# Kernel tuning notes

Measured on AMD Instinct MI355X. Metric: run time of the kernel, lower is better.

The kernel has to match this reference:

```python
import jax, jax.numpy as jnp
import numpy as np


def setup_inputs() -> dict:
    key = jax.random.key(0)
    k1, k2 = jax.random.split(key)
    B, C, H, W = 1, 256, 96, 96
    C8 = C // 8
    x = jax.random.normal(k1, (B, C, H, W), dtype=jnp.float32)
    # 1x1 conv == per-pixel linear projection; weight [C8, C], bias [C8]
    w_conv = jax.random.normal(k2, (C8, C), dtype=jnp.float32) * (1.0 / np.sqrt(C))
    b_conv = jnp.zeros((C8,), dtype=jnp.float32)
    return {"x": x, "w_conv": w_conv, "b_conv": b_conv}


def reference(x, w_conv, b_conv):
    B, C, H, W = x.shape  # B must be 1 (module constraint)
    C8 = w_conv.shape[0]
    # conv_1: 1x1 conv -> [B, C8, H, W]
    x1 = jnp.einsum('bchw,oc->bohw', x, w_conv) + b_conv[None, :, None, None]
    x1 = x1.reshape(-1, H, W)                      # [C8, H, W] (B=1)
    x2 = x1.transpose(2, 1, 0).reshape(-1, C8)     # [W*H, C8], row idx = w*H + h
    x3 = x1.transpose(0, 2, 1).reshape(-1, W * H)  # [C8, W*H], col idx = w*H + h
    x4 = jax.nn.softmax(x2 @ x3, axis=-1)          # [W*H, W*H]
    x5 = x.reshape(-1, W * H)                      # [C, W*H], col idx = h*W + w
    x6 = jax.nn.softmax(x5 @ x4, axis=-1)          # [C, W*H]
    x7 = x6.reshape(B, C, H, W)
    return jax.nn.softmax(x7 + x, axis=-1)         # softmax over W
```

## Files before the change

kernel.cpp:

```cpp
#include <hip/hip_runtime.h>
#include <math.h>

#define HW 9216
#define NI 18

typedef __attribute__((ext_vector_type(8))) short bf16x8;
typedef __attribute__((ext_vector_type(4))) float f32x4;
typedef unsigned short ushort_t;
typedef unsigned int uint_t;

__device__ __forceinline__ ushort_t f2bf(float f) {
    union { float f; uint_t u; } v; v.f = f;
    uint_t u = v.u + 0x7FFF + ((v.u >> 16) & 1);
    return (ushort_t)(u >> 16);
}

#define BAR() do { asm volatile("s_waitcnt lgkmcnt(0)" ::: "memory"); \
                   __builtin_amdgcn_s_barrier(); } while (0)

__global__ __launch_bounds__(256) void k1_conv(
        const float* __restrict__ x, const float* __restrict__ wc,
        const float* __restrict__ bc, ushort_t* __restrict__ Gbt,
        ushort_t* __restrict__ xtile) {
    __shared__ float wt[256][32];
    __shared__ float red[8][32][33];
    int t = threadIdx.x;
    int jt = blockIdx.x;
    for (int i = t; i < 256 * 32; i += 256) {
        int o = i >> 8, c = i & 255;
        wt[c][o] = wc[i];
    }
    __syncthreads();
    int px = t & 31, cg = t >> 5;
    int n = jt * 32 + px;
    float acc[32];
    #pragma unroll
    for (int o = 0; o < 32; ++o) acc[o] = 0.f;
    int c0 = cg * 32;
    ushort_t* xt_out = &xtile[(size_t)jt * 8192 + px];
    for (int cc = 0; cc < 32; ++cc) {
        int c = c0 + cc;
        float xv = x[c * HW + n];
        xt_out[c * 32] = f2bf(xv);
        #pragma unroll
        for (int o4 = 0; o4 < 8; ++o4) {
            float4 wv = *(const float4*)&wt[c][o4 * 4];
            acc[o4*4+0] = fmaf(wv.x, xv, acc[o4*4+0]);
            acc[o4*4+1] = fmaf(wv.y, xv, acc[o4*4+1]);
            acc[o4*4+2] = fmaf(wv.z, xv, acc[o4*4+2]);
            acc[o4*4+3] = fmaf(wv.w, xv, acc[o4*4+3]);
        }
    }
    #pragma unroll
    for (int o = 0; o < 32; ++o) red[cg][px][o] = acc[o];
    __syncthreads();
    int px2 = t >> 3, o2 = (t & 7) * 4;
    float s[4] = {0.f, 0.f, 0.f, 0.f};
    #pragma unroll
    for (int g = 0; g < 8; ++g) {
        s[0] += red[g][px2][o2 + 0];
        s[1] += red[g][px2][o2 + 1];
        s[2] += red[g][px2][o2 + 2];
        s[3] += red[g][px2][o2 + 3];
    }
    int n2 = jt * 32 + px2;
    int h = n2 / 96, w = n2 % 96;
    int p = w * 96 + h;
    uint2 pk;
    pk.x = (uint_t)f2bf(s[0] + bc[o2+0]) | ((uint_t)f2bf(s[1] + bc[o2+1]) << 16);
    pk.y = (uint_t)f2bf(s[2] + bc[o2+2]) | ((uint_t)f2bf(s[3] + bc[o2+3]) << 16);
    *(uint2*)&Gbt[p * 32 + o2] = pk;
}

__global__ __launch_bounds__(512) void k2_stats(
        const ushort_t* __restrict__ Gbt, float* __restrict__ m_part,
        float* __restrict__ l_part) {
    __shared__ float mred[2][64], lred[2][64];
    int t = threadIdx.x;
    int w = t >> 6, l = t & 63;
    int l15 = l & 15, lg = l >> 4;
    int jb = blockIdx.x % 144, qs = blockIdx.x / 144;
    int j0 = jb * 64;
    int rf = w & 3, qp = w >> 2;
    bf16x8 aj = *(const bf16x8*)&Gbt[(j0 + rf * 16 + l15) * 32 + lg * 8];
    float m[4], lsum[4];
    #pragma unroll
    for (int r = 0; r < 4; ++r) { m[r] = -INFINITY; lsum[r] = 0.f; }
    int qbeg = qs * 1152;
    for (int tq = 0; tq < 18; ++tq) {
        int q0 = qbeg + tq * 64;
        bf16x8 b0 = *(const bf16x8*)&Gbt[(q0 + qp * 32 + l15) * 32 + lg * 8];
        bf16x8 b1 = *(const bf16x8*)&Gbt[(q0 + qp * 32 + 16 + l15) * 32 + lg * 8];
        f32x4 s0 = {0.f,0.f,0.f,0.f}, s1 = {0.f,0.f,0.f,0.f};
        s0 = __builtin_amdgcn_mfma_f32_16x16x32_bf16(aj, b0, s0, 0, 0, 0);
        s1 = __builtin_amdgcn_mfma_f32_16x16x32_bf16(aj, b1, s1, 0, 0, 0);
        #pragma unroll
        for (int r = 0; r < 4; ++r) {
            float tm = fmaxf(s0[r], s1[r]);
            float nm = fmaxf(m[r], tm);
            lsum[r] = lsum[r] * __expf(m[r] - nm)
                    + __expf(s0[r] - nm) + __expf(s1[r] - nm);
            m[r] = nm;
        }
    }
    #pragma unroll
    for (int off = 1; off < 16; off <<= 1) {
        #pragma unroll
        for (int r = 0; r < 4; ++r) {
            float mo = __shfl_xor(m[r], off);
            float lo = __shfl_xor(lsum[r], off);
            float nm = fmaxf(m[r], mo);
            lsum[r] = lsum[r] * __expf(m[r] - nm) + lo * __expf(mo - nm);
            m[r] = nm;
        }
    }
    if (l15 == 0) {
        #pragma unroll
        for (int r = 0; r < 4; ++r) {
            mred[qp][rf * 16 + lg * 4 + r] = m[r];
            lred[qp][rf * 16 + lg * 4 + r] = lsum[r];
        }
    }
    __syncthreads();
    if (t < 64) {
        float m0 = mred[0][t], m1 = mred[1][t];
        float l0 = lred[0][t], l1 = lred[1][t];
        float nm = fmaxf(m0, m1);
        float lv = l0 * __expf(m0 - nm) + l1 * __expf(m1 - nm);
        m_part[qs * HW + j0 + t] = nm;
        l_part[qs * HW + j0 + t] = lv;
    }
}

__global__ __launch_bounds__(256) void k2b_merge(
        const float* __restrict__ m_part, const float* __restrict__ l_part,
        float* __restrict__ mg, float* __restrict__ rlg) {
    int j = blockIdx.x * 256 + threadIdx.x;
    float nm = -INFINITY;
    #pragma unroll
    for (int s = 0; s < 8; ++s) nm = fmaxf(nm, m_part[s * HW + j]);
    float lv = 0.f;
    #pragma unroll
    for (int s = 0; s < 8; ++s)
        lv += l_part[s * HW + j] * __expf(m_part[s * HW + j] - nm);
    mg[j] = nm;
    rlg[j] = 1.0f / lv;
}

__global__ __launch_bounds__(256) void kzero(float* __restrict__ Z) {
    int i = blockIdx.x * 256 + threadIdx.x;
    *(float4*)&Z[i * 4] = make_float4(0.f, 0.f, 0.f, 0.f);
}

__device__ __forceinline__ void phaseA2(
        bf16x8 ap0, bf16x8 ap1, bf16x8 bqA, int p0, int pr0,
        ushort_t* __restrict__ pb, int qc, int l15, int lg,
        const float* __restrict__ mg, const float* __restrict__ rlg) {
    f32x4 s0 = {0.f,0.f,0.f,0.f}, s1 = {0.f,0.f,0.f,0.f};
    s0 = __builtin_amdgcn_mfma_f32_16x16x32_bf16(ap0, bqA, s0, 0, 0, 0);
    s1 = __builtin_amdgcn_mfma_f32_16x16x32_bf16(ap1, bqA, s1, 0, 0, 0);
    int prow0 = p0 + pr0 * 16 + lg * 4;
    int prow1 = prow0 + 16;
    float4 m0 = *(const float4*)&mg[prow0], r0 = *(const float4*)&rlg[prow0];
    float4 m1 = *(const float4*)&mg[prow1], r1 = *(const float4*)&rlg[prow1];
    uint2 pk0, pk1;
    pk0.x = (uint_t)f2bf(__expf(s0[0] - m0.x) * r0.x)
          | ((uint_t)f2bf(__expf(s0[1] - m0.y) * r0.y) << 16);
    pk0.y = (uint_t)f2bf(__expf(s0[2] - m0.z) * r0.z)
          | ((uint_t)f2bf(__expf(s0[3] - m0.w) * r0.w) << 16);
    pk1.x = (uint_t)f2bf(__expf(s1[0] - m1.x) * r1.x)
          | ((uint_t)f2bf(__expf(s1[1] - m1.y) * r1.y) << 16);
    pk1.y = (uint_t)f2bf(__expf(s1[2] - m1.z) * r1.z)
          | ((uint_t)f2bf(__expf(s1[3] - m1.w) * r1.w) << 16);
    ushort_t* row = pb + (qc * 16 + l15) * 72;
    *(uint2*)&row[pr0 * 16 + lg * 4]      = pk0;
    *(uint2*)&row[pr0 * 16 + 16 + lg * 4] = pk1;
}

__global__ __launch_bounds__(512) void k3_pv(
        const ushort_t* __restrict__ xtile, const ushort_t* __restrict__ Gbt,
        const float* __restrict__ mg, const float* __restrict__ rlg,
        float* __restrict__ Z) {
    __shared__ ushort_t Pbt[2][64][72];
    int t = threadIdx.x;
    int w = t >> 6, l = t & 63;
    int l15 = l & 15, lg = l >> 4;
    int qb = blockIdx.x % 144, ps = blockIdx.x / 144;
    int q0 = qb * 64;
    int cg = w & 3, qh = w >> 2;
    int qc = w & 3, pr0 = (w >> 2) * 2;
    bf16x8 bqA = *(const bf16x8*)&Gbt[(q0 + qc * 16 + l15) * 32 + lg * 8];
    f32x4 acc[4][2];
    #pragma unroll
    for (int ci = 0; ci < 4; ++ci)
        #pragma unroll
        for (int qs = 0; qs < 2; ++qs) acc[ci][qs] = (f32x4){0.f,0.f,0.f,0.f};
    int tile0 = ps * (NI * 2);
    int p0beg = ps * (NI * 64);
    {
        bf16x8 ap0 = *(const bf16x8*)&Gbt[(p0beg + pr0 * 16 + l15) * 32 + lg * 8];
        bf16x8 ap1 = *(const bf16x8*)&Gbt[(p0beg + pr0 * 16 + 16 + l15) * 32 + lg * 8];
        phaseA2(ap0, ap1, bqA, p0beg, pr0, &Pbt[0][0][0], qc, l15, lg, mg, rlg);
    }
    bf16x8 apc0 = *(const bf16x8*)&Gbt[(p0beg + 64 + pr0 * 16 + l15) * 32 + lg * 8];
    bf16x8 apc1 = *(const bf16x8*)&Gbt[(p0beg + 64 + pr0 * 16 + 16 + l15) * 32 + lg * 8];
    BAR();

    for (int pt = 0; pt < NI; ++pt) {
        int buf = pt & 1;
        const ushort_t* xt0 =
            &xtile[((size_t)(tile0 + pt * 2) * 256 + cg * 64 + l15) * 32 + lg * 8];
        bf16x8 a00 = *(const bf16x8*)&xt0[0];
        bf16x8 a01 = *(const bf16x8*)&xt0[16 * 32];
        bf16x8 a02 = *(const bf16x8*)&xt0[32 * 32];
        bf16x8 a03 = *(const bf16x8*)&xt0[48 * 32];
        const ushort_t* xt1 = xt0 + 8192;
        bf16x8 a10 = *(const bf16x8*)&xt1[0];
        bf16x8 a11 = *(const bf16x8*)&xt1[16 * 32];
        bf16x8 a12 = *(const bf16x8*)&xt1[32 * 32];
        bf16x8 a13 = *(const bf16x8*)&xt1[48 * 32];
        bf16x8 b00 = *(const bf16x8*)&Pbt[buf][qh * 32 + l15][lg * 8];
        bf16x8 b01 = *(const bf16x8*)&Pbt[buf][qh * 32 + l15][32 + lg * 8];
        bf16x8 b10 = *(const bf16x8*)&Pbt[buf][qh * 32 + 16 + l15][lg * 8];
        bf16x8 b11 = *(const bf16x8*)&Pbt[buf][qh * 32 + 16 + l15][32 + lg * 8];
        if (pt < NI - 1) {
            int p0n = p0beg + (pt + 1) * 64;
            phaseA2(apc0, apc1, bqA, p0n, pr0, &Pbt[buf ^ 1][0][0],
                    qc, l15, lg, mg, rlg);
            int p0nn = p0beg + ((pt < NI - 2) ? (pt + 2) : (NI - 1)) * 64;
            apc0 = *(const bf16x8*)&Gbt[(p0nn + pr0 * 16 + l15) * 32 + lg * 8];
            apc1 = *(const bf16x8*)&Gbt[(p0nn + pr0 * 16 + 16 + l15) * 32 + lg * 8];
        }
        acc[0][0] = __builtin_amdgcn_mfma_f32_16x16x32_bf16(a00, b00, acc[0][0], 0,0,0);
        acc[1][0] = __builtin_amdgcn_mfma_f32_16x16x32_bf16(a01, b00, acc[1][0], 0,0,0);
        acc[2][0] = __builtin_amdgcn_mfma_f32_16x16x32_bf16(a02, b00, acc[2][0], 0,0,0);
        acc[3][0] = __builtin_amdgcn_mfma_f32_16x16x32_bf16(a03, b00, acc[3][0], 0,0,0);
        acc[0][1] = __builtin_amdgcn_mfma_f32_16x16x32_bf16(a00, b10, acc[0][1], 0,0,0);
        acc[1][1] = __builtin_amdgcn_mfma_f32_16x16x32_bf16(a01, b10, acc[1][1], 0,0,0);
        acc[2][1] = __builtin_amdgcn_mfma_f32_16x16x32_bf16(a02, b10, acc[2][1], 0,0,0);
        acc[3][1] = __builtin_amdgcn_mfma_f32_16x16x32_bf16(a03, b10, acc[3][1], 0,0,0);
        acc[0][0] = __builtin_amdgcn_mfma_f32_16x16x32_bf16(a10, b01, acc[0][0], 0,0,0);
        acc[1][0] = __builtin_amdgcn_mfma_f32_16x16x32_bf16(a11, b01, acc[1][0], 0,0,0);
        acc[2][0] = __builtin_amdgcn_mfma_f32_16x16x32_bf16(a12, b01, acc[2][0], 0,0,0);
        acc[3][0] = __builtin_amdgcn_mfma_f32_16x16x32_bf16(a13, b01, acc[3][0], 0,0,0);
        acc[0][1] = __builtin_amdgcn_mfma_f32_16x16x32_bf16(a10, b11, acc[0][1], 0,0,0);
        acc[1][1] = __builtin_amdgcn_mfma_f32_16x16x32_bf16(a11, b11, acc[1][1], 0,0,0);
        acc[2][1] = __builtin_amdgcn_mfma_f32_16x16x32_bf16(a12, b11, acc[2][1], 0,0,0);
        acc[3][1] = __builtin_amdgcn_mfma_f32_16x16x32_bf16(a13, b11, acc[3][1], 0,0,0);
        BAR();
    }
    int qcol = q0 + qh * 32 + l15;
    #pragma unroll
    for (int ci = 0; ci < 4; ++ci) {
        int crow = cg * 64 + ci * 16 + lg * 4;
        #pragma unroll
        for (int r = 0; r < 4; ++r) {
            float* zr = &Z[(size_t)(crow + r) * HW + qcol];
            atomicAdd(zr,      acc[ci][0][r]);
            atomicAdd(zr + 16, acc[ci][1][r]);
        }
    }
}

__global__ __launch_bounds__(512) void k4_softmax(
        const float* __restrict__ x, float* __restrict__ ZO) {
    __shared__ float zrow[HW];
    __shared__ float red[8];
    int t = threadIdx.x, c = blockIdx.x;
    int lane = t & 63, wid = t >> 6;
    const float* Zr = &ZO[(size_t)c * HW];
    float lm = -INFINITY;
    #pragma unroll
    for (int k = 0; k < 18; ++k) {
        float v = Zr[t + 512 * k];
        zrow[t + 512 * k] = v;
        lm = fmaxf(lm, v);
    }
    #pragma unroll
    for (int off = 32; off; off >>= 1) lm = fmaxf(lm, __shfl_xor(lm, off));
    if (lane == 0) red[wid] = lm;
    __syncthreads();
    float M = fmaxf(fmaxf(fmaxf(red[0], red[1]), fmaxf(red[2], red[3])),
                    fmaxf(fmaxf(red[4], red[5]), fmaxf(red[6], red[7])));
    __syncthreads();
    float ls = 0.f;
    #pragma unroll
    for (int k = 0; k < 18; ++k) {
        int i = t + 512 * k;
        float e = __expf(zrow[i] - M);
        zrow[i] = e;
        ls += e;
    }
    #pragma unroll
    for (int off = 32; off; off >>= 1) ls += __shfl_xor(ls, off);
    if (lane == 0) red[wid] = ls;
    __syncthreads();
    float rS = 1.0f / (red[0] + red[1] + red[2] + red[3]
                     + red[4] + red[5] + red[6] + red[7]);
    const float* xr = &x[(size_t)c * HW];
    float* outr = &ZO[(size_t)c * HW];
    for (int kk = 0; kk < 12; ++kk) {
        int h = wid + kk * 8;
        int base = h * 96;
        float v0 = fmaf(zrow[base + lane], rS, xr[base + lane]);
        float v1 = (lane < 32)
                 ? fmaf(zrow[base + 64 + lane], rS, xr[base + 64 + lane])
                 : -INFINITY;
        float mm = fmaxf(v0, v1);
        #pragma unroll
        for (int off = 32; off; off >>= 1) mm = fmaxf(mm, __shfl_xor(mm, off));
        float e0 = __expf(v0 - mm);
        float e1 = (lane < 32) ? __expf(v1 - mm) : 0.f;
        float ss = e0 + e1;
        #pragma unroll
        for (int off = 32; off; off >>= 1) ss += __shfl_xor(ss, off);
        float r = 1.0f / ss;
        outr[base + lane] = e0 * r;
        if (lane < 32) outr[base + 64 + lane] = e1 * r;
    }
}

extern "C" void kernel_launch(void* const* d_in, const int* in_sizes, int n_in,
                              void* d_out, int out_size, void* d_ws, size_t ws_size,
                              hipStream_t stream) {
    const float* x  = (const float*)d_in[0];
    const float* wc = (const float*)d_in[1];
    const float* bc = (const float*)d_in[2];
    float* Z = (float*)d_out;

    float* m_part = (float*)d_ws;
    float* l_part = m_part + 8 * HW;
    float* mg     = l_part + 8 * HW;
    float* rlg    = mg + HW;
    ushort_t* xtile = (ushort_t*)(rlg + HW);
    ushort_t* Gbt   = xtile + 256 * HW;

    k1_conv   <<<288,  256, 0, stream>>>(x, wc, bc, Gbt, xtile);
    k2_stats  <<<1152, 512, 0, stream>>>(Gbt, m_part, l_part);
    k2b_merge <<<36,   256, 0, stream>>>(m_part, l_part, mg, rlg);
    kzero     <<<2304, 256, 0, stream>>>(Z);
    k3_pv     <<<1152, 512, 0, stream>>>(xtile, Gbt, mg, rlg, Z);
    k4_softmax<<<256,  512, 0, stream>>>(x, Z);
}
```

Baseline: 235.7 us.

## Make PV kernel warp-private with barrier-free P tiles and folded softmax scale

The PV kernel now uses 256-thread blocks of 4 waves, each covering 32 query columns. Each wave builds its own P tile in a private LDS slot, so the per-iteration block barriers and the double buffer go away. The softmax max and reciprocal-sum are folded into a single log2-domain offset, so P needs one fma plus exp2 and a packed bf16 convert instruction. The custom zero kernel is replaced with hipMemsetAsync. In exchange, the QK^T recomputation per block doubles (each wave recomputes all 64 p rows for its 32 q columns), the grid doubles, and x-tile loads are duplicated across more blocks.

```diff
diff --git a/kernel.cpp b/kernel.cpp
--- a/kernel.cpp
+++ b/kernel.cpp
@@ -3,6 +3,7 @@
 
 #define HW 9216
 #define NI 18
+#define PROW 72
 
 typedef __attribute__((ext_vector_type(8))) short bf16x8;
 typedef __attribute__((ext_vector_type(4))) float f32x4;
@@ -15,8 +16,15 @@
     return (ushort_t)(u >> 16);
 }
 
-#define BAR() do { asm volatile("s_waitcnt lgkmcnt(0)" ::: "memory"); \
-                   __builtin_amdgcn_s_barrier(); } while (0)
+__device__ __forceinline__ uint_t cvtpk_bf16(float lo, float hi) {
+    uint_t r;
+    asm("v_cvt_pk_bf16_f32 %0, %1, %2" : "=v"(r) : "v"(lo), "v"(hi));
+    return r;
+}
+
+__device__ __forceinline__ float pexp(float s, float mu) {
+    return exp2f(fmaf(s, 1.44269504f, mu));
+}
 
 __global__ __launch_bounds__(256) void k1_conv(
         const float* __restrict__ x, const float* __restrict__ wc,
@@ -134,7 +142,7 @@
 
 __global__ __launch_bounds__(256) void k2b_merge(
         const float* __restrict__ m_part, const float* __restrict__ l_part,
-        float* __restrict__ mg, float* __restrict__ rlg) {
+        float* __restrict__ muS) {
     int j = blockIdx.x * 256 + threadIdx.x;
     float nm = -INFINITY;
     #pragma unroll
@@ -143,119 +151,102 @@
     #pragma unroll
     for (int s = 0; s < 8; ++s)
         lv += l_part[s * HW + j] * __expf(m_part[s * HW + j] - nm);
-    mg[j] = nm;
-    rlg[j] = 1.0f / lv;
-}
-
-__global__ __launch_bounds__(256) void kzero(float* __restrict__ Z) {
-    int i = blockIdx.x * 256 + threadIdx.x;
-    *(float4*)&Z[i * 4] = make_float4(0.f, 0.f, 0.f, 0.f);
-}
-
-__device__ __forceinline__ void phaseA2(
-        bf16x8 ap0, bf16x8 ap1, bf16x8 bqA, int p0, int pr0,
-        ushort_t* __restrict__ pb, int qc, int l15, int lg,
-        const float* __restrict__ mg, const float* __restrict__ rlg) {
-    f32x4 s0 = {0.f,0.f,0.f,0.f}, s1 = {0.f,0.f,0.f,0.f};
-    s0 = __builtin_amdgcn_mfma_f32_16x16x32_bf16(ap0, bqA, s0, 0, 0, 0);
-    s1 = __builtin_amdgcn_mfma_f32_16x16x32_bf16(ap1, bqA, s1, 0, 0, 0);
-    int prow0 = p0 + pr0 * 16 + lg * 4;
-    int prow1 = prow0 + 16;
-    float4 m0 = *(const float4*)&mg[prow0], r0 = *(const float4*)&rlg[prow0];
-    float4 m1 = *(const float4*)&mg[prow1], r1 = *(const float4*)&rlg[prow1];
-    uint2 pk0, pk1;
-    pk0.x = (uint_t)f2bf(__expf(s0[0] - m0.x) * r0.x)
-          | ((uint_t)f2bf(__expf(s0[1] - m0.y) * r0.y) << 16);
-    pk0.y = (uint_t)f2bf(__expf(s0[2] - m0.z) * r0.z)
-          | ((uint_t)f2bf(__expf(s0[3] - m0.w) * r0.w) << 16);
-    pk1.x = (uint_t)f2bf(__expf(s1[0] - m1.x) * r1.x)
-          | ((uint_t)f2bf(__expf(s1[1] - m1.y) * r1.y) << 16);
-    pk1.y = (uint_t)f2bf(__expf(s1[2] - m1.z) * r1.z)
-          | ((uint_t)f2bf(__expf(s1[3] - m1.w) * r1.w) << 16);
-    ushort_t* row = pb + (qc * 16 + l15) * 72;
-    *(uint2*)&row[pr0 * 16 + lg * 4]      = pk0;
-    *(uint2*)&row[pr0 * 16 + 16 + lg * 4] = pk1;
-}
-
-__global__ __launch_bounds__(512) void k3_pv(
+    muS[j] = -(nm + logf(lv)) * 1.44269504f;
+}
+
+__global__ __launch_bounds__(256, 4) void k3_pv(
         const ushort_t* __restrict__ xtile, const ushort_t* __restrict__ Gbt,
-        const float* __restrict__ mg, const float* __restrict__ rlg,
-        float* __restrict__ Z) {
-    __shared__ ushort_t Pbt[2][64][72];
-    int t = threadIdx.x;
-    int w = t >> 6, l = t & 63;
-    int l15 = l & 15, lg = l >> 4;
-    int qb = blockIdx.x % 144, ps = blockIdx.x / 144;
-    int q0 = qb * 64;
-    int cg = w & 3, qh = w >> 2;
-    int qc = w & 3, pr0 = (w >> 2) * 2;
-    bf16x8 bqA = *(const bf16x8*)&Gbt[(q0 + qc * 16 + l15) * 32 + lg * 8];
+        const float* __restrict__ muS, float* __restrict__ Z) {
+    __shared__ ushort_t Pw[4][32][PROW];
+    const int t = threadIdx.x;
+    const int w = t >> 6;
+    const int l15 = t & 15, lg = (t >> 4) & 3;
+    const int qb = blockIdx.x % 288, ps = blockIdx.x / 288;
+    const int q0 = qb * 32;
+    const int cbase = w * 64;
+
+    bf16x8 bq0 = *(const bf16x8*)&Gbt[(q0 + l15) * 32 + lg * 8];
+    bf16x8 bq1 = *(const bf16x8*)&Gbt[(q0 + 16 + l15) * 32 + lg * 8];
+
     f32x4 acc[4][2];
     #pragma unroll
-    for (int ci = 0; ci < 4; ++ci)
-        #pragma unroll
-        for (int qs = 0; qs < 2; ++qs) acc[ci][qs] = (f32x4){0.f,0.f,0.f,0.f};
-    int tile0 = ps * (NI * 2);
-    int p0beg = ps * (NI * 64);
-    {
-        bf16x8 ap0 = *(const bf16x8*)&Gbt[(p0beg + pr0 * 16 + l15) * 32 + lg * 8];
-        bf16x8 ap1 = *(const bf16x8*)&Gbt[(p0beg + pr0 * 16 + 16 + l15) * 32 + lg * 8];
-        phaseA2(ap0, ap1, bqA, p0beg, pr0, &Pbt[0][0][0], qc, l15, lg, mg, rlg);
-    }
-    bf16x8 apc0 = *(const bf16x8*)&Gbt[(p0beg + 64 + pr0 * 16 + l15) * 32 + lg * 8];
-    bf16x8 apc1 = *(const bf16x8*)&Gbt[(p0beg + 64 + pr0 * 16 + 16 + l15) * 32 + lg * 8];
-    BAR();
-
-    for (int pt = 0; pt < NI; ++pt) {
-        int buf = pt & 1;
-        const ushort_t* xt0 =
-            &xtile[((size_t)(tile0 + pt * 2) * 256 + cg * 64 + l15) * 32 + lg * 8];
-        bf16x8 a00 = *(const bf16x8*)&xt0[0];
-        bf16x8 a01 = *(const bf16x8*)&xt0[16 * 32];
-        bf16x8 a02 = *(const bf16x8*)&xt0[32 * 32];
-        bf16x8 a03 = *(const bf16x8*)&xt0[48 * 32];
-        const ushort_t* xt1 = xt0 + 8192;
-        bf16x8 a10 = *(const bf16x8*)&xt1[0];
-        bf16x8 a11 = *(const bf16x8*)&xt1[16 * 32];
-        bf16x8 a12 = *(const bf16x8*)&xt1[32 * 32];
-        bf16x8 a13 = *(const bf16x8*)&xt1[48 * 32];
-        bf16x8 b00 = *(const bf16x8*)&Pbt[buf][qh * 32 + l15][lg * 8];
-        bf16x8 b01 = *(const bf16x8*)&Pbt[buf][qh * 32 + l15][32 + lg * 8];
-        bf16x8 b10 = *(const bf16x8*)&Pbt[buf][qh * 32 + 16 + l15][lg * 8];
-        bf16x8 b11 = *(const bf16x8*)&Pbt[buf][qh * 32 + 16 + l15][32 + lg * 8];
-        if (pt < NI - 1) {
-            int p0n = p0beg + (pt + 1) * 64;
-            phaseA2(apc0, apc1, bqA, p0n, pr0, &Pbt[buf ^ 1][0][0],
-                    qc, l15, lg, mg, rlg);
-            int p0nn = p0beg + ((pt < NI - 2) ? (pt + 2) : (NI - 1)) * 64;
-            apc0 = *(const bf16x8*)&Gbt[(p0nn + pr0 * 16 + l15) * 32 + lg * 8];
-            apc1 = *(const bf16x8*)&Gbt[(p0nn + pr0 * 16 + 16 + l15) * 32 + lg * 8];
-        }
-        acc[0][0] = __builtin_amdgcn_mfma_f32_16x16x32_bf16(a00, b00, acc[0][0], 0,0,0);
-        acc[1][0] = __builtin_amdgcn_mfma_f32_16x16x32_bf16(a01, b00, acc[1][0], 0,0,0);
-        acc[2][0] = __builtin_amdgcn_mfma_f32_16x16x32_bf16(a02, b00, acc[2][0], 0,0,0);
-        acc[3][0] = __builtin_amdgcn_mfma_f32_16x16x32_bf16(a03, b00, acc[3][0], 0,0,0);
-        acc[0][1] = __builtin_amdgcn_mfma_f32_16x16x32_bf16(a00, b10, acc[0][1], 0,0,0);
-        acc[1][1] = __builtin_amdgcn_mfma_f32_16x16x32_bf16(a01, b10, acc[1][1], 0,0,0);
-        acc[2][1] = __builtin_amdgcn_mfma_f32_16x16x32_bf16(a02, b10, acc[2][1], 0,0,0);
-        acc[3][1] = __builtin_amdgcn_mfma_f32_16x16x32_bf16(a03, b10, acc[3][1], 0,0,0);
-        acc[0][0] = __builtin_amdgcn_mfma_f32_16x16x32_bf16(a10, b01, acc[0][0], 0,0,0);
-        acc[1][0] = __builtin_amdgcn_mfma_f32_16x16x32_bf16(a11, b01, acc[1][0], 0,0,0);
-        acc[2][0] = __builtin_amdgcn_mfma_f32_16x16x32_bf16(a12, b01, acc[2][0], 0,0,0);
-        acc[3][0] = __builtin_amdgcn_mfma_f32_16x16x32_bf16(a13, b01, acc[3][0], 0,0,0);
-        acc[0][1] = __builtin_amdgcn_mfma_f32_16x16x32_bf16(a10, b11, acc[0][1], 0,0,0);
-        acc[1][1] = __builtin_amdgcn_mfma_f32_16x16x32_bf16(a11, b11, acc[1][1], 0,0,0);
-        acc[2][1] = __builtin_amdgcn_mfma_f32_16x16x32_bf16(a12, b11, acc[2][1], 0,0,0);
-        acc[3][1] = __builtin_amdgcn_mfma_f32_16x16x32_bf16(a13, b11, acc[3][1], 0,0,0);
-        BAR();
-    }
-    int qcol = q0 + qh * 32 + l15;
-    #pragma unroll
     for (int ci = 0; ci < 4; ++ci) {
-        int crow = cg * 64 + ci * 16 + lg * 4;
+        acc[ci][0] = (f32x4){0.f,0.f,0.f,0.f};
+        acc[ci][1] = (f32x4){0.f,0.f,0.f,0.f};
+    }
+
+    const int p0beg = ps * (NI * 64);
+    const int tile0 = ps * (NI * 2);
+    ushort_t* pw = &Pw[w][0][0];
+
+    bf16x8 ap[4];
+    #pragma unroll
+    for (int pm = 0; pm < 4; ++pm)
+        ap[pm] = *(const bf16x8*)&Gbt[(p0beg + pm * 16 + l15) * 32 + lg * 8];
+
+    for (int it = 0; it < NI; ++it) {
+        const int p0 = p0beg + it * 64;
+        const ushort_t* xa =
+            &xtile[((size_t)(tile0 + 2 * it) * 256 + cbase + l15) * 32 + lg * 8];
+        bf16x8 a0[4];
+        #pragma unroll
+        for (int ci = 0; ci < 4; ++ci)
+            a0[ci] = *(const bf16x8*)&xa[ci * 512];
+
+        f32x4 s[4][2];
+        #pragma unroll
+        for (int pm = 0; pm < 4; ++pm) {
+            f32x4 z = {0.f,0.f,0.f,0.f};
+            s[pm][0] = __builtin_amdgcn_mfma_f32_16x16x32_bf16(ap[pm], bq0, z, 0,0,0);
+            s[pm][1] = __builtin_amdgcn_mfma_f32_16x16x32_bf16(ap[pm], bq1, z, 0,0,0);
+        }
+        if (it < NI - 1) {
+            const int pn = p0 + 64;
+            #pragma unroll
+            for (int pm = 0; pm < 4; ++pm)
+                ap[pm] = *(const bf16x8*)&Gbt[(pn + pm * 16 + l15) * 32 + lg * 8];
+        }
+        #pragma unroll
+        for (int pm = 0; pm < 4; ++pm) {
+            float4 mu = *(const float4*)&muS[p0 + pm * 16 + lg * 4];
+            #pragma unroll
+            for (int qn = 0; qn < 2; ++qn) {
+                uint2 u;
+                u.x = cvtpk_bf16(pexp(s[pm][qn][0], mu.x),
+                                 pexp(s[pm][qn][1], mu.y));
+                u.y = cvtpk_bf16(pexp(s[pm][qn][2], mu.z),
+                                 pexp(s[pm][qn][3], mu.w));
+                *(uint2*)&pw[(qn * 16 + l15) * PROW + pm * 16 + lg * 4] = u;
+            }
+        }
+        bf16x8 a1[4];
+        const ushort_t* xa1 = xa + 8192;
+        #pragma unroll
+        for (int ci = 0; ci < 4; ++ci)
+            a1[ci] = *(const bf16x8*)&xa1[ci * 512];
+
+        bf16x8 b00 = *(const bf16x8*)&pw[l15 * PROW + lg * 8];
+        bf16x8 b01 = *(const bf16x8*)&pw[(16 + l15) * PROW + lg * 8];
+        #pragma unroll
+        for (int ci = 0; ci < 4; ++ci) {
+            acc[ci][0] = __builtin_amdgcn_mfma_f32_16x16x32_bf16(a0[ci], b00, acc[ci][0], 0,0,0);
+            acc[ci][1] = __builtin_amdgcn_mfma_f32_16x16x32_bf16(a0[ci], b01, acc[ci][1], 0,0,0);
+        }
+        bf16x8 b10 = *(const bf16x8*)&pw[l15 * PROW + 32 + lg * 8];
+        bf16x8 b11 = *(const bf16x8*)&pw[(16 + l15) * PROW + 32 + lg * 8];
+        #pragma unroll
+        for (int ci = 0; ci < 4; ++ci) {
+            acc[ci][0] = __builtin_amdgcn_mfma_f32_16x16x32_bf16(a1[ci], b10, acc[ci][0], 0,0,0);
+            acc[ci][1] = __builtin_amdgcn_mfma_f32_16x16x32_bf16(a1[ci], b11, acc[ci][1], 0,0,0);
+        }
+    }
+    const int qc0 = q0 + l15;
+    #pragma unroll
+    for (int ci = 0; ci < 4; ++ci) {
+        const int crow = cbase + ci * 16 + lg * 4;
         #pragma unroll
         for (int r = 0; r < 4; ++r) {
-            float* zr = &Z[(size_t)(crow + r) * HW + qcol];
+            float* zr = &Z[(size_t)(crow + r) * HW + qc0];
             atomicAdd(zr,      acc[ci][0][r]);
             atomicAdd(zr + 16, acc[ci][1][r]);
         }
@@ -330,15 +321,14 @@
 
     float* m_part = (float*)d_ws;
     float* l_part = m_part + 8 * HW;
-    float* mg     = l_part + 8 * HW;
-    float* rlg    = mg + HW;
-    ushort_t* xtile = (ushort_t*)(rlg + HW);
+    float* muS    = l_part + 8 * HW;
+    ushort_t* xtile = (ushort_t*)(muS + HW);
     ushort_t* Gbt   = xtile + 256 * HW;
 
     k1_conv   <<<288,  256, 0, stream>>>(x, wc, bc, Gbt, xtile);
     k2_stats  <<<1152, 512, 0, stream>>>(Gbt, m_part, l_part);
-    k2b_merge <<<36,   256, 0, stream>>>(m_part, l_part, mg, rlg);
-    kzero     <<<2304, 256, 0, stream>>>(Z);
-    k3_pv     <<<1152, 512, 0, stream>>>(xtile, Gbt, mg, rlg, Z);
+    k2b_merge <<<36,   256, 0, stream>>>(m_part, l_part, muS);
+    hipMemsetAsync(Z, 0, (size_t)out_size * sizeof(float), stream);
+    k3_pv     <<<2304, 256, 0, stream>>>(xtile, Gbt, muS, Z);
     k4_softmax<<<256,  512, 0, stream>>>(x, Z);
 }
```

Result: no change. 237.5 us (+0.8%).
